# Performance work log

Measured on AMD Instinct MI355X. Metric: run time of the kernel, lower is better.

Reference implementation:

```python
import jax, jax.numpy as jnp
import numpy as np

EPS = 1e-5


def _conv_w(x, k):
    # cross-correlation along width, kernel size 2, padding 1 -> width W+1
    xp = jnp.pad(x, ((0, 0), (0, 0), (0, 0), (1, 1)))
    return k[0] * xp[..., :-1] + k[1] * xp[..., 1:]


def _conv_h(x, k):
    # cross-correlation along height, kernel size 2, padding 1 -> height H+1
    xp = jnp.pad(x, ((0, 0), (0, 0), (1, 1), (0, 0)))
    return k[0] * xp[..., :-1, :] + k[1] * xp[..., 1:, :]


def _dwt(x, lp, hp):
    L = _conv_h(_conv_w(x, lp), lp)
    Hc = _conv_h(_conv_w(x, hp), hp)
    return L[:, :, ::2, ::2], Hc[:, :, ::2, ::2]


def _bn(y, g, b, m, v):
    # eval-mode batchnorm over channel axis 1
    scale = (g / jnp.sqrt(v + EPS))[None, :, None, None]
    shift = (b - m * g / jnp.sqrt(v + EPS))[None, :, None, None]
    return y * scale + shift


def setup_inputs() -> dict:
    key = jax.random.key(0)
    ks = jax.random.split(key, 8)
    S, B, H, W, C = 5, 8, 512, 512, 64
    x = jax.random.normal(ks[0], (B, 1, H, W), dtype=jnp.float32)
    lp = jnp.tile(jnp.array([0.7071, 0.7071], dtype=jnp.float32), (S, 1))
    hp = jnp.tile(jnp.array([0.7071, -0.7071], dtype=jnp.float32), (S, 1))
    w1 = jax.random.normal(ks[1], (S, C, 1), dtype=jnp.float32) * 0.5
    w2 = jax.random.normal(ks[2], (S, C, C), dtype=jnp.float32) * (1.0 / np.sqrt(C))
    g1 = jnp.ones((S, C), jnp.float32)
    b1 = jnp.zeros((S, C), jnp.float32)
    m1 = jax.random.normal(ks[3], (S, C), dtype=jnp.float32) * 0.1
    v1 = jax.random.uniform(ks[4], (S, C), dtype=jnp.float32) + 0.5
    g2 = jnp.ones((S, C), jnp.float32)
    b2 = jnp.zeros((S, C), jnp.float32)
    m2 = jax.random.normal(ks[5], (S, C), dtype=jnp.float32) * 0.1
    v2 = jax.random.uniform(ks[6], (S, C), dtype=jnp.float32) + 0.5
    return dict(x=x, lp=lp, hp=hp, w1=w1, w2=w2, g1=g1, b1=b1, m1=m1, v1=v1,
                g2=g2, b2=b2, m2=m2, v2=v2)


def reference(x, lp, hp, w1, w2, g1, b1, m1, v1, g2, b2, m2, v2):
    # Returns stacked-over-scale (L, H_coeff, processed_L):
    #   L, Hc: [S, B, 1, H', W'];  P: [S, B, 64, H', W']
    def per_scale(lp_s, hp_s, w1_s, g1_s, b1_s, m1_s, v1_s,
                  w2_s, g2_s, b2_s, m2_s, v2_s):
        L, Hc = _dwt(x, lp_s, hp_s)
        y = jnp.einsum('oc,bchw->bohw', w1_s, L)
        y = jax.nn.relu(_bn(y, g1_s, b1_s, m1_s, v1_s))
        y = jnp.einsum('oc,bchw->bohw', w2_s, y)
        y = jax.nn.relu(_bn(y, g2_s, b2_s, m2_s, v2_s))
        return L, Hc, y

    return jax.vmap(per_scale)(lp, hp, w1, g1, b1, m1, v1, w2, g2, b2, m2, v2)
```

## Files before the change

kernel.cpp:

```cpp
#include <hip/hip_runtime.h>
#include <math.h>

#define EPSF 1e-5f

constexpr int Sn = 5, Bn = 8, Hin = 512, Win = 512, Cn = 64;
constexpr int HO = 257, WO = 257;
constexpr int HW = HO * WO;
constexpr int NPIX = Bn * HW;
constexpr int TOTPIX = Sn * NPIX;
constexpr int NSB = Sn * Bn;
constexpr int HWP = (HW + 3) & ~3;

constexpr unsigned U_TOTPIX = (unsigned)TOTPIX;
constexpr unsigned U_TWOT   = 2u * U_TOTPIX;
constexpr unsigned PTOTu    = (unsigned)((long)NSB * Cn * HW);
constexpr unsigned U_TOT    = U_TWOT + PTOTu;

constexpr int    WSF    = 64 + Cn * 66 * 2;
constexpr size_t LR_OFF = (size_t)Sn * WSF;
constexpr size_t H_OFF  = LR_OFF + (size_t)NSB * HWP * 2;
constexpr size_t WS_NEED = (H_OFF + (size_t)NSB * HWP) * 4;

typedef float f32x4 __attribute__((ext_vector_type(4)));
typedef f32x4 f32x4u __attribute__((aligned(8)));

__global__ __launch_bounds__(64) void precompute_kernel(
    const float* __restrict__ w1, const float* __restrict__ w2,
    const float* __restrict__ g1, const float* __restrict__ b1,
    const float* __restrict__ m1, const float* __restrict__ v1,
    const float* __restrict__ g2, const float* __restrict__ b2,
    const float* __restrict__ m2, const float* __restrict__ v2,
    float* __restrict__ ws) {
    int s = blockIdx.x;
    int c = threadIdx.x;
    __shared__ float sa1[Cn], st1[Cn], stc[Cn], stS[Cn];
    __shared__ int   scS[Cn];

    int idx = s * Cn + c;
    float sc1 = g1[idx] / sqrtf(v1[idx] + EPSF);
    float a1  = sc1 * w1[idx];
    float t1  = b1[idx] - m1[idx] * sc1;
    sa1[c] = a1;
    st1[c] = t1;
    float tc = (a1 != 0.f) ? (-t1 / a1) : INFINITY;
    stc[c] = tc;
    __syncthreads();

    int rk = 0;
    for (int c2 = 0; c2 < Cn; c2++) {
        float t = stc[c2];
        rk += (t < tc) || (t == tc && c2 < c);
    }
    stS[rk] = tc;
    scS[rk] = c;
    __syncthreads();

    float* wss = ws + (size_t)s * WSF;
    wss[c] = stS[c];

    int o = c;
    float sc2 = g2[idx] / sqrtf(v2[idx] + EPSF);
    float t2o = b2[idx] - m2[idx] * sc2;
    const float* w2row = w2 + ((size_t)s * Cn + o) * Cn;

    float alpha = 0.f, beta = t2o;
    for (int cc = 0; cc < Cn; cc++) {
        float a = sa1[cc];
        bool act = (a < 0.f) || (a == 0.f && st1[cc] > 0.f);
        if (act) {
            float wf = sc2 * w2row[cc];
            alpha = fmaf(wf, a, alpha);
            beta  = fmaf(wf, st1[cc], beta);
        }
    }
    float2* abrow = (float2*)(wss + Cn);
    abrow[o * 66 + 0] = make_float2(alpha, beta);

    for (int r = 1; r <= Cn; r++) {
        int cc = scS[r - 1];
        float a = sa1[cc];
        if (a != 0.f) {
            float wf = sc2 * w2row[cc];
            float sgn = (a > 0.f) ? 1.f : -1.f;
            alpha = fmaf(sgn * wf, a, alpha);
            beta  = fmaf(sgn * wf, st1[cc], beta);
        }
        abrow[o * 66 + r] = make_float2(alpha, beta);
    }
}

constexpr int GPT = 4;
constexpr int TPB = 256;
constexpr int PIXPB = TPB * GPT;
constexpr int NCHUNK = (HW + PIXPB - 1) / PIXPB;

__device__ __forceinline__ float pwl(const float2 ab, float v) {
    return fmaxf(fmaf(ab.x, v, ab.y), 0.f);
}

__device__ __forceinline__ void dwt_lh(
    const float* __restrict__ xb, int i, int j,
    float l0, float l1, float h0, float h1,
    float& Lq, float& Hq) {
    const int r0 = 2 * i - 1, r1 = 2 * i;
    const int c0 = 2 * j - 1, c1 = 2 * j;
    const float x00 = (r0 >= 0 && r0 < Hin && c0 >= 0 ) ? xb[r0 * Win + c0] : 0.f;
    const float x01 = (r0 >= 0 && r0 < Hin && c1 < Win) ? xb[r0 * Win + c1] : 0.f;
    const float x10 = (r1 < Hin && c0 >= 0 )            ? xb[r1 * Win + c0] : 0.f;
    const float x11 = (r1 < Hin && c1 < Win)            ? xb[r1 * Win + c1] : 0.f;
    Lq = l0 * (l0 * x00 + l1 * x01) + l1 * (l0 * x10 + l1 * x11);
    Hq = h0 * (h0 * x00 + h1 * x01) + h1 * (h0 * x10 + h1 * x11);
}

__global__ __launch_bounds__(TPB) void dwt_pack(
    const float* __restrict__ x,
    const float* __restrict__ lp, const float* __restrict__ hp,
    const float* __restrict__ ws_tab,
    float* __restrict__ lrws, float* __restrict__ hws) {
    __shared__ float stS[Cn];
    const int tid = threadIdx.x;
    const int b = blockIdx.y, s = blockIdx.z;
    if (tid < Cn) stS[tid] = ws_tab[(size_t)s * WSF + tid];
    __syncthreads();

    const int pbase = (blockIdx.x * TPB + tid) * GPT;
    if (pbase >= HW) return;

    const float l0 = lp[2 * s], l1 = lp[2 * s + 1];
    const float h0 = hp[2 * s], h1 = hp[2 * s + 1];
    const float* xb = x + (size_t)b * (Hin * Win);

    float Lv[GPT], Hv[GPT];
    int   rr[GPT];

    int i = pbase / WO;
    int j = pbase - i * WO;
    #pragma unroll
    for (int q = 0; q < GPT; ++q) {
        if (pbase + q < HW) {
            dwt_lh(xb, i, j, l0, l1, h0, h1, Lv[q], Hv[q]);
            int lo = 0, hi = Cn;
            while (lo < hi) {
                const int mid = (lo + hi) >> 1;
                if (stS[mid] < Lv[q]) lo = mid + 1; else hi = mid;
            }
            rr[q] = lo;
        } else { Lv[q] = 0.f; Hv[q] = 0.f; rr[q] = 0; }
        if (++j == WO) { j = 0; ++i; }
    }

    const int sb = s * Bn + b;
    float2* lr = (float2*)lrws + (size_t)sb * HWP + pbase;
    float*  hp_ = hws + (size_t)sb * HWP + pbase;

    if (pbase + GPT <= HW) {
        f32x4 p01 = f32x4{Lv[0], (float)rr[0], Lv[1], (float)rr[1]};
        f32x4 p23 = f32x4{Lv[2], (float)rr[2], Lv[3], (float)rr[3]};
        *(f32x4*)(lr)     = p01;
        *(f32x4*)(lr + 2) = p23;
        *(f32x4*)(hp_)    = f32x4{Hv[0], Hv[1], Hv[2], Hv[3]};
    } else {
        #pragma unroll
        for (int q = 0; q < GPT; ++q) {
            if (pbase + q < HW) {
                lr[q]  = make_float2(Lv[q], (float)rr[q]);
                hp_[q] = Hv[q];
            }
        }
    }
}

constexpr int EPB = TPB * 16;
constexpr unsigned NBLK2 = (U_TOT + EPB - 1) / EPB;

__global__ __launch_bounds__(TPB) void store_flat(
    const float* __restrict__ ws_tab,
    const float* __restrict__ lrws,
    const float* __restrict__ hws,
    float* __restrict__ out) {
    __shared__ float2 tabs[2][66];

    const int tid = threadIdx.x;
    const unsigned base = (unsigned)blockIdx.x * (unsigned)EPB;
    const float2* LR = (const float2*)lrws;

    if (base + EPB <= U_TOTPIX) {
        #pragma unroll
        for (int k = 0; k < 4; ++k) {
            const unsigned f = base + (unsigned)k * (TPB * 4u) + (unsigned)tid * 4u;
            const unsigned sb  = f / (unsigned)HW;
            const unsigned px0 = f - sb * (unsigned)HW;
            if (px0 <= (unsigned)(HW - 4)) {
                const float2* lr = LR + (size_t)sb * HWP + px0;
                const f32x4u v01 = *(const f32x4u*)(lr);
                const f32x4u v23 = *(const f32x4u*)(lr + 2);
                f32x4 v; v.x = v01.x; v.y = v01.z; v.z = v23.x; v.w = v23.z;
                __builtin_nontemporal_store(v, (f32x4*)(out + f));
            } else {
                #pragma unroll
                for (int e = 0; e < 4; ++e) {
                    const unsigned fe = f + (unsigned)e;
                    const unsigned s2 = fe / (unsigned)HW;
                    const unsigned px = fe - s2 * (unsigned)HW;
                    out[fe] = LR[(size_t)s2 * HWP + px].x;
                }
            }
        }
        return;
    }
    if (base >= U_TOTPIX && base + EPB <= U_TWOT) {
        #pragma unroll
        for (int k = 0; k < 4; ++k) {
            const unsigned f = base + (unsigned)k * (TPB * 4u) + (unsigned)tid * 4u;
            const unsigned g = f - U_TOTPIX;
            const unsigned sb  = g / (unsigned)HW;
            const unsigned px0 = g - sb * (unsigned)HW;
            if (px0 <= (unsigned)(HW - 4)) {
                const float* hp_ = hws + (size_t)sb * HWP + px0;
                f32x4 v; v.x = hp_[0]; v.y = hp_[1]; v.z = hp_[2]; v.w = hp_[3];
                __builtin_nontemporal_store(v, (f32x4*)(out + f));
            } else {
                #pragma unroll
                for (int e = 0; e < 4; ++e) {
                    const unsigned ge = g + (unsigned)e;
                    const unsigned s2 = ge / (unsigned)HW;
                    const unsigned px = ge - s2 * (unsigned)HW;
                    out[U_TOTPIX + ge] = hws[(size_t)s2 * HWP + px];
                }
            }
        }
        return;
    }
    if (base >= U_TWOT && base + EPB <= U_TOT) {
        const unsigned qbase = base - U_TWOT;
        const unsigned plane_first = qbase / (unsigned)HW;
        const unsigned plane_last  = (qbase + (unsigned)(EPB - 1)) / (unsigned)HW;
        if (tid < 132) {
            const int slot = (tid >= 66);
            const int idx  = slot ? tid - 66 : tid;
            const unsigned pl = slot ? plane_last : plane_first;
            const int s = (int)(pl >> 9);
            const int o = (int)(pl & 63u);
            const float2* row =
                (const float2*)(ws_tab + (size_t)s * WSF + Cn) + (size_t)o * 66;
            tabs[slot][idx] = row[idx];
        }
        __syncthreads();

        #pragma unroll
        for (int k = 0; k < 4; ++k) {
            const unsigned q = qbase + (unsigned)k * (TPB * 4u) + (unsigned)tid * 4u;
            const unsigned plane = q / (unsigned)HW;
            const unsigned px0   = q - plane * (unsigned)HW;
            const int row = (plane != plane_first);
            if (px0 <= (unsigned)(HW - 4)) {
                const float2* lr = LR + (size_t)(plane >> 6) * HWP + px0;
                const f32x4u v01 = *(const f32x4u*)(lr);
                const f32x4u v23 = *(const f32x4u*)(lr + 2);
                const float2 ab0 = tabs[row][(int)v01.y];
                const float2 ab1 = tabs[row][(int)v01.w];
                const float2 ab2 = tabs[row][(int)v23.y];
                const float2 ab3 = tabs[row][(int)v23.w];
                f32x4 v;
                v.x = pwl(ab0, v01.x);
                v.y = pwl(ab1, v01.z);
                v.z = pwl(ab2, v23.x);
                v.w = pwl(ab3, v23.z);
                __builtin_nontemporal_store(v, (f32x4*)(out + U_TWOT + q));
            } else {
                #pragma unroll
                for (int e = 0; e < 4; ++e) {
                    const unsigned qe = q + (unsigned)e;
                    const unsigned pl = qe / (unsigned)HW;
                    const unsigned px = qe - pl * (unsigned)HW;
                    const int rw = (pl != plane_first);
                    const float2 lrv = LR[(size_t)(pl >> 6) * HWP + px];
                    const float2 ab  = tabs[rw][(int)lrv.y];
                    out[U_TWOT + qe] = pwl(ab, lrv.x);
                }
            }
        }
        return;
    }
    for (int k = 0; k < 16; ++k) {
        const unsigned f = base + (unsigned)k * (unsigned)TPB + (unsigned)tid;
        if (f >= U_TOT) return;
        if (f < U_TOTPIX) {
            const unsigned sb = f / (unsigned)HW;
            const unsigned px = f - sb * (unsigned)HW;
            out[f] = LR[(size_t)sb * HWP + px].x;
        } else if (f < U_TWOT) {
            const unsigned g  = f - U_TOTPIX;
            const unsigned sb = g / (unsigned)HW;
            const unsigned px = g - sb * (unsigned)HW;
            out[f] = hws[(size_t)sb * HWP + px];
        } else {
            const unsigned q  = f - U_TWOT;
            const unsigned pl = q / (unsigned)HW;
            const unsigned px = q - pl * (unsigned)HW;
            const int s = (int)(pl >> 9);
            const int o = (int)(pl & 63u);
            const float2 lrv = LR[(size_t)(pl >> 6) * HWP + px];
            const float2 ab  = ((const float2*)(ws_tab + (size_t)s * WSF + Cn))
                                   [(size_t)o * 66 + (int)lrv.y];
            out[f] = pwl(ab, lrv.x);
        }
    }
}

__global__ __launch_bounds__(TPB) void dwt_halo(
    const float* __restrict__ x,
    const float* __restrict__ lp, const float* __restrict__ hp,
    float* __restrict__ Lout, float* __restrict__ Hout) {
    const int tid = threadIdx.x;
    const int b = blockIdx.y, s = blockIdx.z;

    const float l0 = lp[2 * s], l1 = lp[2 * s + 1];
    const float h0 = hp[2 * s], h1 = hp[2 * s + 1];
    const float* xb = x + (size_t)b * (Hin * Win);

    const int pbase = (blockIdx.x * TPB + tid) * GPT;
    if (pbase >= HW) return;

    float Lv[GPT + 3], Hv[GPT + 3];
    int i = pbase / WO;
    int j = pbase - i * WO;
    #pragma unroll
    for (int q = 0; q < GPT; ++q) {
        dwt_lh(xb, i, j, l0, l1, h0, h1, Lv[q], Hv[q]);
        if (++j == WO) { j = 0; ++i; }
    }
    Lv[4] = __shfl_down(Lv[0], 1, 64);  Hv[4] = __shfl_down(Hv[0], 1, 64);
    Lv[5] = __shfl_down(Lv[1], 1, 64);  Hv[5] = __shfl_down(Hv[1], 1, 64);
    Lv[6] = __shfl_down(Lv[2], 1, 64);  Hv[6] = __shfl_down(Hv[2], 1, 64);
    if ((tid & 63) == 63) {
        #pragma unroll
        for (int q = GPT; q < GPT + 3; ++q) {
            dwt_lh(xb, i, j, l0, l1, h0, h1, Lv[q], Hv[q]);
            if (++j == WO) { j = 0; ++i; }
        }
    }

    const int sb = s * Bn + b;
    const size_t lb = (size_t)sb * HW + pbase;
    const int dlt = (4 - (sb & 3)) & 3;
    const bool fast = (pbase + GPT + 3 <= HW);

    if (fast) {
        f32x4 l4, h4;
        switch (dlt) {
            case 0:  l4 = f32x4{Lv[0], Lv[1], Lv[2], Lv[3]};
                     h4 = f32x4{Hv[0], Hv[1], Hv[2], Hv[3]}; break;
            case 1:  l4 = f32x4{Lv[1], Lv[2], Lv[3], Lv[4]};
                     h4 = f32x4{Hv[1], Hv[2], Hv[3], Hv[4]}; break;
            case 2:  l4 = f32x4{Lv[2], Lv[3], Lv[4], Lv[5]};
                     h4 = f32x4{Hv[2], Hv[3], Hv[4], Hv[5]}; break;
            default: l4 = f32x4{Lv[3], Lv[4], Lv[5], Lv[6]};
                     h4 = f32x4{Hv[3], Hv[4], Hv[5], Hv[6]}; break;
        }
        *(f32x4*)(Lout + lb + dlt) = l4;
        __builtin_nontemporal_store(h4, (f32x4*)(Hout + lb + dlt));
        if (pbase == 0) {
            if (dlt > 0) { Lout[lb + 0] = Lv[0]; Hout[lb + 0] = Hv[0]; }
            if (dlt > 1) { Lout[lb + 1] = Lv[1]; Hout[lb + 1] = Hv[1]; }
            if (dlt > 2) { Lout[lb + 2] = Lv[2]; Hout[lb + 2] = Hv[2]; }
        }
    } else {
        #pragma unroll
        for (int q = 0; q < GPT; ++q) {
            if (pbase + q < HW) {
                Lout[lb + q] = Lv[q];
                Hout[lb + q] = Hv[q];
            }
        }
    }
}

__global__ __launch_bounds__(TPB) void pstore_v5(
    const float* __restrict__ Lin,
    const float* __restrict__ ws,
    float* __restrict__ Pout) {
    __shared__ float  stS[Cn];
    __shared__ float2 sab[4 * 66];

    const int tid = threadIdx.x;
    const int og  = blockIdx.y;
    const int sb  = blockIdx.z;
    const int s   = sb >> 3;

    const float* wss = ws + (size_t)s * WSF;
    if (tid < Cn) stS[tid] = wss[tid];
    const float2* abg = (const float2*)(wss + Cn) + (size_t)og * 4 * 66;
    for (int t = tid; t < 4 * 66; t += TPB) sab[t] = abg[t];
    __syncthreads();

    const int p4 = (blockIdx.x * TPB + tid) * GPT;
    const float* Lp = Lin + (size_t)sb * HW;

    float Lv[GPT + 3];
    int   lo7[GPT + 3];

    #pragma unroll
    for (int q = 0; q < GPT; ++q) {
        const int px = p4 + q;
        const float Lq = (px < HW) ? Lp[px] : 0.f;
        Lv[q] = Lq;
        int lo = 0, hi = Cn;
        while (lo < hi) {
            const int mid = (lo + hi) >> 1;
            if (stS[mid] < Lq) lo = mid + 1; else hi = mid;
        }
        lo7[q] = lo;
    }
    Lv[4] = __shfl_down(Lv[0], 1, 64);  lo7[4] = __shfl_down(lo7[0], 1, 64);
    Lv[5] = __shfl_down(Lv[1], 1, 64);  lo7[5] = __shfl_down(lo7[1], 1, 64);
    Lv[6] = __shfl_down(Lv[2], 1, 64);  lo7[6] = __shfl_down(lo7[2], 1, 64);
    if ((tid & 63) == 63) {
        #pragma unroll
        for (int q = GPT; q < GPT + 3; ++q) {
            const int px = p4 + q;
            const float Lq = (px < HW) ? Lp[px] : 0.f;
            Lv[q] = Lq;
            int lo = 0, hi = Cn;
            while (lo < hi) {
                const int mid = (lo + hi) >> 1;
                if (stS[mid] < Lq) lo = mid + 1; else hi = mid;
            }
            lo7[q] = lo;
        }
    }

    float* const Pb = Pout + ((size_t)sb * Cn + (size_t)og * 4) * HW;

    if (p4 + GPT + 3 <= HW) {
        {   f32x4 v = f32x4{pwl(sab[0 * 66 + lo7[0]], Lv[0]),
                            pwl(sab[0 * 66 + lo7[1]], Lv[1]),
                            pwl(sab[0 * 66 + lo7[2]], Lv[2]),
                            pwl(sab[0 * 66 + lo7[3]], Lv[3])};
            *(f32x4*)(Pb + p4) = v; }
        {   f32x4 v = f32x4{pwl(sab[1 * 66 + lo7[3]], Lv[3]),
                            pwl(sab[1 * 66 + lo7[4]], Lv[4]),
                            pwl(sab[1 * 66 + lo7[5]], Lv[5]),
                            pwl(sab[1 * 66 + lo7[6]], Lv[6])};
            *(f32x4*)(Pb + (size_t)HW + p4 + 3) = v; }
        {   f32x4 v = f32x4{pwl(sab[2 * 66 + lo7[2]], Lv[2]),
                            pwl(sab[2 * 66 + lo7[3]], Lv[3]),
                            pwl(sab[2 * 66 + lo7[4]], Lv[4]),
                            pwl(sab[2 * 66 + lo7[5]], Lv[5])};
            *(f32x4*)(Pb + 2 * (size_t)HW + p4 + 2) = v; }
        {   f32x4 v = f32x4{pwl(sab[3 * 66 + lo7[1]], Lv[1]),
                            pwl(sab[3 * 66 + lo7[2]], Lv[2]),
                            pwl(sab[3 * 66 + lo7[3]], Lv[3]),
                            pwl(sab[3 * 66 + lo7[4]], Lv[4])};
            *(f32x4*)(Pb + 3 * (size_t)HW + p4 + 1) = v; }
        if (p4 == 0) {
            Pb[1 * (size_t)HW + 0] = pwl(sab[1 * 66 + lo7[0]], Lv[0]);
            Pb[1 * (size_t)HW + 1] = pwl(sab[1 * 66 + lo7[1]], Lv[1]);
            Pb[1 * (size_t)HW + 2] = pwl(sab[1 * 66 + lo7[2]], Lv[2]);
            Pb[2 * (size_t)HW + 0] = pwl(sab[2 * 66 + lo7[0]], Lv[0]);
            Pb[2 * (size_t)HW + 1] = pwl(sab[2 * 66 + lo7[1]], Lv[1]);
            Pb[3 * (size_t)HW + 0] = pwl(sab[3 * 66 + lo7[0]], Lv[0]);
        }
    } else {
        #pragma unroll
        for (int q = 0; q < GPT; ++q) {
            const int px = p4 + q;
            if (px >= HW) break;
            const float Lq = Lv[q];
            const int   r  = lo7[q];
            Pb[0 * (size_t)HW + px] = pwl(sab[0 * 66 + r], Lq);
            Pb[1 * (size_t)HW + px] = pwl(sab[1 * 66 + r], Lq);
            Pb[2 * (size_t)HW + px] = pwl(sab[2 * 66 + r], Lq);
            Pb[3 * (size_t)HW + px] = pwl(sab[3 * 66 + r], Lq);
        }
    }
}

extern "C" void kernel_launch(void* const* d_in, const int* in_sizes, int n_in,
                              void* d_out, int out_size, void* d_ws, size_t ws_size,
                              hipStream_t stream) {
    const float* x  = (const float*)d_in[0];
    const float* lp = (const float*)d_in[1];
    const float* hp = (const float*)d_in[2];
    const float* w1 = (const float*)d_in[3];
    const float* w2 = (const float*)d_in[4];
    const float* g1 = (const float*)d_in[5];
    const float* b1 = (const float*)d_in[6];
    const float* m1 = (const float*)d_in[7];
    const float* v1 = (const float*)d_in[8];
    const float* g2 = (const float*)d_in[9];
    const float* b2 = (const float*)d_in[10];
    const float* m2 = (const float*)d_in[11];
    const float* v2 = (const float*)d_in[12];

    float* out  = (float*)d_out;
    float* Lout = out;
    float* Hout = out + TOTPIX;
    float* Pout = out + 2 * TOTPIX;
    float* ws   = (float*)d_ws;

    precompute_kernel<<<Sn, Cn, 0, stream>>>(w1, w2, g1, b1, m1, v1,
                                             g2, b2, m2, v2, ws);

    dim3 grid1(NCHUNK, Bn, Sn);

    if (ws_size >= WS_NEED) {
        float* lrws = ws + LR_OFF;
        float* hws  = ws + H_OFF;
        dwt_pack<<<grid1, TPB, 0, stream>>>(x, lp, hp, ws, lrws, hws);
        store_flat<<<dim3(NBLK2), TPB, 0, stream>>>(ws, lrws, hws, out);
    } else {
        dwt_halo<<<grid1, TPB, 0, stream>>>(x, lp, hp, Lout, Hout);
        dim3 grid2(NCHUNK, Cn / 4, Sn * Bn);
        pstore_v5<<<grid2, TPB, 0, stream>>>(Lout, ws, Pout);
    }
}
```

Baseline: 733.1 us.

## Pack L value and segment index into one 32-bit word in workspace

The DWT pass now stores each L coefficient and its piecewise-linear segment index in a single 32-bit word, with the index in the low 7 mantissa bits, instead of a float2 pair. This halves the intermediate bytes written and then re-read by the flat store kernel. The store kernel also replaces per-element integer divisions with a plane-boundary comparison and an offset. In exchange, the stored L output loses its low 7 mantissa bits, a small precision loss on the returned L values.

Result: no change. 743.1 us (+1.4%).

```diff
diff --git a/kernel.cpp b/kernel.cpp
--- a/kernel.cpp
+++ b/kernel.cpp
@@ -17,12 +17,14 @@
 constexpr unsigned U_TOT    = U_TWOT + PTOTu;
 
 constexpr int    WSF    = 64 + Cn * 66 * 2;
-constexpr size_t LR_OFF = (size_t)Sn * WSF;
-constexpr size_t H_OFF  = LR_OFF + (size_t)NSB * HWP * 2;
+constexpr size_t PK_OFF = (size_t)Sn * WSF;
+constexpr size_t H_OFF  = PK_OFF + (size_t)NSB * HWP;
 constexpr size_t WS_NEED = (H_OFF + (size_t)NSB * HWP) * 4;
 
-typedef float f32x4 __attribute__((ext_vector_type(4)));
-typedef f32x4 f32x4u __attribute__((aligned(8)));
+typedef float    f32x4  __attribute__((ext_vector_type(4)));
+typedef unsigned u32x4  __attribute__((ext_vector_type(4)));
+typedef u32x4 u32x4a4 __attribute__((aligned(4)));
+typedef f32x4 f32x4a4 __attribute__((aligned(4)));
 
 __global__ __launch_bounds__(64) void precompute_kernel(
     const float* __restrict__ w1, const float* __restrict__ w2,
@@ -116,7 +118,7 @@
     const float* __restrict__ x,
     const float* __restrict__ lp, const float* __restrict__ hp,
     const float* __restrict__ ws_tab,
-    float* __restrict__ lrws, float* __restrict__ hws) {
+    unsigned* __restrict__ pkws, float* __restrict__ hws) {
     __shared__ float stS[Cn];
     const int tid = threadIdx.x;
     const int b = blockIdx.y, s = blockIdx.z;
@@ -130,42 +132,37 @@
     const float h0 = hp[2 * s], h1 = hp[2 * s + 1];
     const float* xb = x + (size_t)b * (Hin * Win);
 
-    float Lv[GPT], Hv[GPT];
-    int   rr[GPT];
+    float    Hv[GPT];
+    unsigned pk[GPT];
 
     int i = pbase / WO;
     int j = pbase - i * WO;
     #pragma unroll
     for (int q = 0; q < GPT; ++q) {
         if (pbase + q < HW) {
-            dwt_lh(xb, i, j, l0, l1, h0, h1, Lv[q], Hv[q]);
+            float Lq;
+            dwt_lh(xb, i, j, l0, l1, h0, h1, Lq, Hv[q]);
             int lo = 0, hi = Cn;
             while (lo < hi) {
                 const int mid = (lo + hi) >> 1;
-                if (stS[mid] < Lv[q]) lo = mid + 1; else hi = mid;
+                if (stS[mid] < Lq) lo = mid + 1; else hi = mid;
             }
-            rr[q] = lo;
-        } else { Lv[q] = 0.f; Hv[q] = 0.f; rr[q] = 0; }
+            pk[q] = (__float_as_uint(Lq) & ~127u) | (unsigned)lo;
+        } else { pk[q] = 0u; Hv[q] = 0.f; }
         if (++j == WO) { j = 0; ++i; }
     }
 
     const int sb = s * Bn + b;
-    float2* lr = (float2*)lrws + (size_t)sb * HWP + pbase;
-    float*  hp_ = hws + (size_t)sb * HWP + pbase;
+    unsigned* pp = pkws + (size_t)sb * HWP + pbase;
+    float*    hp_ = hws + (size_t)sb * HWP + pbase;
 
     if (pbase + GPT <= HW) {
-        f32x4 p01 = f32x4{Lv[0], (float)rr[0], Lv[1], (float)rr[1]};
-        f32x4 p23 = f32x4{Lv[2], (float)rr[2], Lv[3], (float)rr[3]};
-        *(f32x4*)(lr)     = p01;
-        *(f32x4*)(lr + 2) = p23;
-        *(f32x4*)(hp_)    = f32x4{Hv[0], Hv[1], Hv[2], Hv[3]};
+        *(u32x4*)(pp)  = u32x4{pk[0], pk[1], pk[2], pk[3]};
+        *(f32x4*)(hp_) = f32x4{Hv[0], Hv[1], Hv[2], Hv[3]};
     } else {
         #pragma unroll
         for (int q = 0; q < GPT; ++q) {
-            if (pbase + q < HW) {
-                lr[q]  = make_float2(Lv[q], (float)rr[q]);
-                hp_[q] = Hv[q];
-            }
+            if (pbase + q < HW) { pp[q] = pk[q]; hp_[q] = Hv[q]; }
         }
     }
 }
@@ -175,57 +172,59 @@
 
 __global__ __launch_bounds__(TPB) void store_flat(
     const float* __restrict__ ws_tab,
-    const float* __restrict__ lrws,
+    const unsigned* __restrict__ pkws,
     const float* __restrict__ hws,
     float* __restrict__ out) {
     __shared__ float2 tabs[2][66];
 
     const int tid = threadIdx.x;
     const unsigned base = (unsigned)blockIdx.x * (unsigned)EPB;
-    const float2* LR = (const float2*)lrws;
 
     if (base + EPB <= U_TOTPIX) {
+        const unsigned sb0 = base / (unsigned)HW;
+        const unsigned bnd = (sb0 + 1u) * (unsigned)HW;
         #pragma unroll
         for (int k = 0; k < 4; ++k) {
             const unsigned f = base + (unsigned)k * (TPB * 4u) + (unsigned)tid * 4u;
-            const unsigned sb  = f / (unsigned)HW;
-            const unsigned px0 = f - sb * (unsigned)HW;
-            if (px0 <= (unsigned)(HW - 4)) {
-                const float2* lr = LR + (size_t)sb * HWP + px0;
-                const f32x4u v01 = *(const f32x4u*)(lr);
-                const f32x4u v23 = *(const f32x4u*)(lr + 2);
-                f32x4 v; v.x = v01.x; v.y = v01.z; v.z = v23.x; v.w = v23.z;
+            const unsigned sb = sb0 + (f >= bnd);
+            const size_t idx = (size_t)f + 3u * sb;
+            if (f + 3u < bnd || f >= bnd) {
+                const u32x4a4 w = *(const u32x4a4*)(pkws + idx);
+                f32x4 v;
+                v.x = __uint_as_float(w.x); v.y = __uint_as_float(w.y);
+                v.z = __uint_as_float(w.z); v.w = __uint_as_float(w.w);
                 __builtin_nontemporal_store(v, (f32x4*)(out + f));
             } else {
                 #pragma unroll
                 for (int e = 0; e < 4; ++e) {
                     const unsigned fe = f + (unsigned)e;
-                    const unsigned s2 = fe / (unsigned)HW;
-                    const unsigned px = fe - s2 * (unsigned)HW;
-                    out[fe] = LR[(size_t)s2 * HWP + px].x;
+                    const unsigned s2 = sb0 + (fe >= bnd);
+                    out[fe] = __uint_as_float(pkws[(size_t)fe + 3u * s2]);
                 }
             }
         }
         return;
     }
     if (base >= U_TOTPIX && base + EPB <= U_TWOT) {
+        const unsigned gbase = base - U_TOTPIX;
+        const unsigned sb0 = gbase / (unsigned)HW;
+        const unsigned bnd = (sb0 + 1u) * (unsigned)HW;
         #pragma unroll
         for (int k = 0; k < 4; ++k) {
             const unsigned f = base + (unsigned)k * (TPB * 4u) + (unsigned)tid * 4u;
             const unsigned g = f - U_TOTPIX;
-            const unsigned sb  = g / (unsigned)HW;
-            const unsigned px0 = g - sb * (unsigned)HW;
-            if (px0 <= (unsigned)(HW - 4)) {
-                const float* hp_ = hws + (size_t)sb * HWP + px0;
-                f32x4 v; v.x = hp_[0]; v.y = hp_[1]; v.z = hp_[2]; v.w = hp_[3];
-                __builtin_nontemporal_store(v, (f32x4*)(out + f));
+            const unsigned sb = sb0 + (g >= bnd);
+            const size_t idx = (size_t)g + 3u * sb;
+            if (g + 3u < bnd || g >= bnd) {
+                const f32x4a4 v = *(const f32x4a4*)(hws + idx);
+                f32x4 vv; vv.x = v.x; vv.y = v.y; vv.z = v.z; vv.w = v.w;
+                __builtin_nontemporal_store(vv, (f32x4*)(out + f));
             } else {
                 #pragma unroll
                 for (int e = 0; e < 4; ++e) {
                     const unsigned ge = g + (unsigned)e;
-                    const unsigned s2 = ge / (unsigned)HW;
-                    const unsigned px = ge - s2 * (unsigned)HW;
-                    out[U_TOTPIX + ge] = hws[(size_t)s2 * HWP + px];
+                    const unsigned s2 = sb0 + (ge >= bnd);
+                    out[U_TOTPIX + ge] = hws[(size_t)ge + 3u * s2];
                 }
             }
         }
@@ -233,50 +232,49 @@
     }
     if (base >= U_TWOT && base + EPB <= U_TOT) {
         const unsigned qbase = base - U_TWOT;
-        const unsigned plane_first = qbase / (unsigned)HW;
-        const unsigned plane_last  = (qbase + (unsigned)(EPB - 1)) / (unsigned)HW;
+        const unsigned pf  = qbase / (unsigned)HW;
+        const unsigned bnd = (pf + 1u) * (unsigned)HW;
+        const unsigned plast = (qbase + (unsigned)(EPB - 1)) / (unsigned)HW;
+        long off0 = (long)((pf      >> 6) * (size_t)HWP) - (long)pf        * HW;
+        long off1 = (long)((plast   >> 6) * (size_t)HWP) - (long)plast     * HW;
         if (tid < 132) {
             const int slot = (tid >= 66);
-            const int idx  = slot ? tid - 66 : tid;
-            const unsigned pl = slot ? plane_last : plane_first;
+            const int iidx = slot ? tid - 66 : tid;
+            const unsigned pl = slot ? plast : pf;
             const int s = (int)(pl >> 9);
             const int o = (int)(pl & 63u);
             const float2* row =
                 (const float2*)(ws_tab + (size_t)s * WSF + Cn) + (size_t)o * 66;
-            tabs[slot][idx] = row[idx];
+            tabs[slot][iidx] = row[iidx];
         }
         __syncthreads();
 
         #pragma unroll
         for (int k = 0; k < 4; ++k) {
             const unsigned q = qbase + (unsigned)k * (TPB * 4u) + (unsigned)tid * 4u;
-            const unsigned plane = q / (unsigned)HW;
-            const unsigned px0   = q - plane * (unsigned)HW;
-            const int row = (plane != plane_first);
-            if (px0 <= (unsigned)(HW - 4)) {
-                const float2* lr = LR + (size_t)(plane >> 6) * HWP + px0;
-                const f32x4u v01 = *(const f32x4u*)(lr);
-                const f32x4u v23 = *(const f32x4u*)(lr + 2);
-                const float2 ab0 = tabs[row][(int)v01.y];
-                const float2 ab1 = tabs[row][(int)v01.w];
-                const float2 ab2 = tabs[row][(int)v23.y];
-                const float2 ab3 = tabs[row][(int)v23.w];
+            const int row = (q >= bnd);
+            if (q + 3u < bnd || q >= bnd) {
+                const size_t idx = (size_t)((long)q + (row ? off1 : off0));
+                const u32x4a4 w = *(const u32x4a4*)(pkws + idx);
+                const float2 ab0 = tabs[row][w.x & 127u];
+                const float2 ab1 = tabs[row][w.y & 127u];
+                const float2 ab2 = tabs[row][w.z & 127u];
+                const float2 ab3 = tabs[row][w.w & 127u];
                 f32x4 v;
-                v.x = pwl(ab0, v01.x);
-                v.y = pwl(ab1, v01.z);
-                v.z = pwl(ab2, v23.x);
-                v.w = pwl(ab3, v23.z);
+                v.x = pwl(ab0, __uint_as_float(w.x));
+                v.y = pwl(ab1, __uint_as_float(w.y));
+                v.z = pwl(ab2, __uint_as_float(w.z));
+                v.w = pwl(ab3, __uint_as_float(w.w));
                 __builtin_nontemporal_store(v, (f32x4*)(out + U_TWOT + q));
             } else {
                 #pragma unroll
                 for (int e = 0; e < 4; ++e) {
                     const unsigned qe = q + (unsigned)e;
-                    const unsigned pl = qe / (unsigned)HW;
-                    const unsigned px = qe - pl * (unsigned)HW;
-                    const int rw = (pl != plane_first);
-                    const float2 lrv = LR[(size_t)(pl >> 6) * HWP + px];
-                    const float2 ab  = tabs[rw][(int)lrv.y];
-                    out[U_TWOT + qe] = pwl(ab, lrv.x);
+                    const int rw = (qe >= bnd);
+                    const size_t idx = (size_t)((long)qe + (rw ? off1 : off0));
+                    const unsigned w = pkws[idx];
+                    const float2 ab = tabs[rw][w & 127u];
+                    out[U_TWOT + qe] = pwl(ab, __uint_as_float(w));
                 }
             }
         }
@@ -288,7 +286,7 @@
         if (f < U_TOTPIX) {
             const unsigned sb = f / (unsigned)HW;
             const unsigned px = f - sb * (unsigned)HW;
-            out[f] = LR[(size_t)sb * HWP + px].x;
+            out[f] = __uint_as_float(pkws[(size_t)sb * HWP + px]);
         } else if (f < U_TWOT) {
             const unsigned g  = f - U_TOTPIX;
             const unsigned sb = g / (unsigned)HW;
@@ -300,10 +298,10 @@
             const unsigned px = q - pl * (unsigned)HW;
             const int s = (int)(pl >> 9);
             const int o = (int)(pl & 63u);
-            const float2 lrv = LR[(size_t)(pl >> 6) * HWP + px];
+            const unsigned w = pkws[(size_t)(pl >> 6) * HWP + px];
             const float2 ab  = ((const float2*)(ws_tab + (size_t)s * WSF + Cn))
-                                   [(size_t)o * 66 + (int)lrv.y];
-            out[f] = pwl(ab, lrv.x);
+                                   [(size_t)o * 66 + (int)(w & 127u)];
+            out[f] = pwl(ab, __uint_as_float(w));
         }
     }
 }
@@ -505,10 +503,10 @@
     dim3 grid1(NCHUNK, Bn, Sn);
 
     if (ws_size >= WS_NEED) {
-        float* lrws = ws + LR_OFF;
-        float* hws  = ws + H_OFF;
-        dwt_pack<<<grid1, TPB, 0, stream>>>(x, lp, hp, ws, lrws, hws);
-        store_flat<<<dim3(NBLK2), TPB, 0, stream>>>(ws, lrws, hws, out);
+        unsigned* pkws = (unsigned*)(ws + PK_OFF);
+        float*    hws  = ws + H_OFF;
+        dwt_pack<<<grid1, TPB, 0, stream>>>(x, lp, hp, ws, pkws, hws);
+        store_flat<<<dim3(NBLK2), TPB, 0, stream>>>(ws, pkws, hws, out);
     } else {
         dwt_halo<<<grid1, TPB, 0, stream>>>(x, lp, hp, Lout, Hout);
         dim3 grid2(NCHUNK, Cn / 4, Sn * Bn);
```
